# Optimization experiments

Hardware: AMD Instinct MI355X
Metric: run time of the kernel (lower is better)

## Reference

```python
import jax, jax.numpy as jnp
import numpy as np

N = 100000
E = 1600000
IN = 256
H = 4
C = 64


def setup_inputs() -> dict:
    key = jax.random.key(0)
    k1, k2, k3, k4, k5, k6 = jax.random.split(key, 6)
    x = jax.random.normal(k1, (N, IN), dtype=jnp.float32)
    edge_index = jax.random.randint(k2, (2, E), 0, N, dtype=jnp.int64)
    W = jax.random.normal(k3, (IN, H * C), dtype=jnp.float32) * (1.0 / np.sqrt(IN))
    att_src = jax.random.normal(k4, (H, C), dtype=jnp.float32) * 0.1
    att_dst = jax.random.normal(k5, (H, C), dtype=jnp.float32) * 0.1
    bias = jax.random.normal(k6, (H * C,), dtype=jnp.float32) * 0.01
    return {"x": x, "edge_index": edge_index, "W": W, "att_src": att_src, "att_dst": att_dst, "bias": bias}


def reference(x, edge_index, W, att_src, att_dst, bias):
    n = x.shape[0]
    # PyG GATConv default: add self-loops
    loops = jnp.arange(n, dtype=edge_index.dtype)
    src = jnp.concatenate([edge_index[0], loops])  # [E+N]
    dst = jnp.concatenate([edge_index[1], loops])  # [E+N]
    xp = (x @ W).reshape(n, H, C)                   # [N,H,C]
    a_src = jnp.einsum('nhc,hc->nh', xp, att_src)   # [N,H]
    a_dst = jnp.einsum('nhc,hc->nh', xp, att_dst)   # [N,H]
    # per-edge attention logits, LeakyReLU(0.2)
    alpha = jax.nn.leaky_relu(a_src[src] + a_dst[dst], negative_slope=0.2)  # [E+N,H]
    # segment softmax over destination neighborhoods (every node has a self-loop)
    amax = jax.ops.segment_max(alpha, dst, num_segments=n)
    amax = jnp.where(jnp.isfinite(amax), amax, 0.0)
    ex = jnp.exp(alpha - amax[dst])
    denom = jax.ops.segment_sum(ex, dst, num_segments=n)
    w = ex / denom[dst]                              # [E+N,H]
    # weighted scatter-add of source features
    msg = xp[src] * w[..., None]                     # [E+N,H,C]
    agg = jax.ops.segment_sum(msg, dst, num_segments=n)  # [N,H,C]
    out = agg.reshape(n, H * C) + bias
    return jax.nn.elu(out)
```

## Files before the change

### kernel.cpp

```cpp
#include <hip/hip_runtime.h>
#include <hip/hip_fp16.h>

#define FDIM 256
#define NH 4

typedef float f32x4 __attribute__((ext_vector_type(4)));
typedef short short8v __attribute__((ext_vector_type(8)));
typedef unsigned short ushort_t;
typedef unsigned short ushort8 __attribute__((ext_vector_type(8)));
typedef unsigned short ushort4v __attribute__((ext_vector_type(4)));

__device__ __forceinline__ float leaky02(float v) { return v > 0.0f ? v : 0.2f * v; }

__device__ __forceinline__ ushort_t f2bf(float f) {
    union { float f; unsigned int u; } v; v.f = f;
    unsigned int u = v.u + 0x7FFFu + ((v.u >> 16) & 1u);
    return (ushort_t)(u >> 16);
}

__device__ __forceinline__ float bf2f(ushort_t u) {
    union { float f; unsigned int u; } v;
    v.u = ((unsigned int)u) << 16;
    return v.f;
}

__device__ __forceinline__ void gload_lds16(const void* g, void* lds) {
    __builtin_amdgcn_global_load_lds((const __attribute__((address_space(1))) unsigned int*)g,
                                     (__attribute__((address_space(3))) unsigned int*)lds, 16, 0, 0);
}

__device__ __forceinline__ float recw(const int4& r, int h) {
    unsigned v = (h < 2) ? (unsigned)r.y : (unsigned)r.z;
    unsigned bits = (h & 1) ? (v >> 16) : (v & 0xFFFFu);
    __half_raw hr; hr.x = (unsigned short)bits;
    return __half2float(*reinterpret_cast<__half*>(&hr));
}

__global__ __launch_bounds__(256) void wprep_kernel(const float* __restrict__ W,
                                                    ushort_t* __restrict__ Wbf) {
    const int k = blockIdx.x;
    const int col = threadIdx.x;
    Wbf[(((size_t)(k >> 3) * 256 + col) << 3) + (k & 7)] = f2bf(W[(size_t)k * 256 + col]);
}

__global__ __launch_bounds__(512) void gemm_xp_kernel(const float* __restrict__ x,
                                                      const ushort_t* __restrict__ Wbf,
                                                      const float* __restrict__ att_s,
                                                      const float* __restrict__ att_d,
                                                      ushort_t* __restrict__ xpb,
                                                      float* __restrict__ a_src,
                                                      float* __restrict__ a_dst, int n) {
    __shared__ ushort_t a_lds[4096];
    __shared__ ushort_t b_lds[8192];
    const int t = threadIdx.x;
    const int w = t >> 6, l = t & 63;
    const int wm = w >> 2, wn = w & 3;
    const int row0 = blockIdx.x << 7;
    const int fr = l & 15, fk = l >> 4;

    const int arow = t & 127, akb = t >> 7;
    int grow = row0 + arow;
    if (grow >= n) grow = n - 1;
    const float* aptr = x + (size_t)grow * FDIM + (akb << 3);

    f32x4 acc[4][4] = {};

    for (int s = 0; s < 8; ++s) {
        float4 v0 = *(const float4*)(aptr + s * 32);
        float4 v1 = *(const float4*)(aptr + s * 32 + 4);
        ushort8 u;
        u[0]=f2bf(v0.x); u[1]=f2bf(v0.y); u[2]=f2bf(v0.z); u[3]=f2bf(v0.w);
        u[4]=f2bf(v1.x); u[5]=f2bf(v1.y); u[6]=f2bf(v1.z); u[7]=f2bf(v1.w);

        if (s) __syncthreads();

        *(ushort8*)&a_lds[(((size_t)akb << 7) + arow) << 3] = u;
        gload_lds16(Wbf + (size_t)s * 8192 + ((size_t)t << 3), (char*)b_lds + (w << 10));
        gload_lds16(Wbf + (size_t)s * 8192 + ((size_t)(t + 512) << 3), (char*)b_lds + 8192 + (w << 10));
        __syncthreads();

        short8v af[4], bfv[4];
        #pragma unroll
        for (int m = 0; m < 4; ++m)
            af[m] = *(const short8v*)&a_lds[(((size_t)fk << 7) + wm * 64 + m * 16 + fr) << 3];
        #pragma unroll
        for (int nf = 0; nf < 4; ++nf)
            bfv[nf] = *(const short8v*)&b_lds[(((size_t)fk << 8) + wn * 64 + nf * 16 + fr) << 3];
        #pragma unroll
        for (int m = 0; m < 4; ++m)
            #pragma unroll
            for (int nf = 0; nf < 4; ++nf)
                acc[m][nf] = __builtin_amdgcn_mfma_f32_16x16x32_bf16(af[m], bfv[nf], acc[m][nf], 0, 0, 0);
    }

    #pragma unroll
    for (int m = 0; m < 4; ++m) {
        const int r_ = row0 + wm * 64 + m * 16 + fk * 4;
        #pragma unroll
        for (int nf = 0; nf < 4; ++nf) {
            const int c_ = wn * 64 + nf * 16 + fr;
            #pragma unroll
            for (int j = 0; j < 4; ++j)
                if (r_ + j < n)
                    xpb[(size_t)(r_ + j) * FDIM + c_] = f2bf(acc[m][nf][j]);
        }
    }

    float att_sv[4], att_dv[4];
    #pragma unroll
    for (int nf = 0; nf < 4; ++nf) {
        att_sv[nf] = att_s[(wn << 6) + (nf << 4) + fr];
        att_dv[nf] = att_d[(wn << 6) + (nf << 4) + fr];
    }
    #pragma unroll
    for (int m = 0; m < 4; ++m) {
        #pragma unroll
        for (int j = 0; j < 4; ++j) {
            float ps = acc[m][0][j] * att_sv[0] + acc[m][1][j] * att_sv[1]
                     + acc[m][2][j] * att_sv[2] + acc[m][3][j] * att_sv[3];
            float pd = acc[m][0][j] * att_dv[0] + acc[m][1][j] * att_dv[1]
                     + acc[m][2][j] * att_dv[2] + acc[m][3][j] * att_dv[3];
            ps += __shfl_xor(ps, 1, 64); pd += __shfl_xor(pd, 1, 64);
            ps += __shfl_xor(ps, 2, 64); pd += __shfl_xor(pd, 2, 64);
            ps += __shfl_xor(ps, 4, 64); pd += __shfl_xor(pd, 4, 64);
            ps += __shfl_xor(ps, 8, 64); pd += __shfl_xor(pd, 8, 64);
            if (fr == 0) {
                const int r_ = row0 + wm * 64 + m * 16 + fk * 4 + j;
                if (r_ < n) {
                    a_src[r_ * NH + wn] = ps;
                    a_dst[r_ * NH + wn] = pd;
                }
            }
        }
    }
}

__global__ void degree_kernel(const int* __restrict__ dst, int* __restrict__ counts, int E) {
    int stride = gridDim.x * blockDim.x;
    for (int e = blockIdx.x * blockDim.x + threadIdx.x; e < E; e += stride)
        atomicAdd(&counts[dst[e]], 1);
}

__global__ __launch_bounds__(256) void scan_partial_kernel(const int* __restrict__ counts,
                                                           int* __restrict__ blockSums, int n) {
    __shared__ int sdata[256];
    const int b = blockIdx.x, t = threadIdx.x;
    const int base = b * 1024 + t * 4;
    int s = 0;
    #pragma unroll
    for (int j = 0; j < 4; ++j)
        if (base + j < n) s += counts[base + j];
    sdata[t] = s;
    __syncthreads();
    for (int off = 128; off > 0; off >>= 1) {
        if (t < off) sdata[t] += sdata[t + off];
        __syncthreads();
    }
    if (t == 0) blockSums[b] = sdata[0];
}

__global__ __launch_bounds__(256) void scan_blocksums_kernel(const int* __restrict__ blockSums,
                                                             int* __restrict__ blockOffs, int nb) {
    __shared__ int s[256];
    const int t = threadIdx.x;
    int v = (t < nb) ? blockSums[t] : 0;
    s[t] = v;
    __syncthreads();
    for (int d = 1; d < 256; d <<= 1) {
        int u = (t >= d) ? s[t - d] : 0;
        __syncthreads();
        s[t] += u;
        __syncthreads();
    }
    if (t < nb) blockOffs[t] = s[t] - v;
}

__global__ __launch_bounds__(256) void scan_final_kernel(const int* __restrict__ counts,
                                                         const int* __restrict__ blockOffs,
                                                         int* __restrict__ offsets,
                                                         int* __restrict__ cursor, int n) {
    __shared__ int s[256];
    const int b = blockIdx.x, t = threadIdx.x;
    const int base = b * 1024 + t * 4;
    int c[4];
    int tsum = 0;
    #pragma unroll
    for (int j = 0; j < 4; ++j) {
        c[j] = (base + j < n) ? counts[base + j] : 0;
        tsum += c[j];
    }
    s[t] = tsum;
    __syncthreads();
    for (int d = 1; d < 256; d <<= 1) {
        int u = (t >= d) ? s[t - d] : 0;
        __syncthreads();
        s[t] += u;
        __syncthreads();
    }
    int run = s[t] - tsum + blockOffs[b];
    #pragma unroll
    for (int j = 0; j < 4; ++j) {
        if (base + j < n) {
            offsets[base + j] = run;
            cursor[base + j] = run;
            run += c[j];
        }
    }
}

__global__ void scatter_kernel(const int* __restrict__ src, const int* __restrict__ dst,
                               const float* __restrict__ a_src, const float* __restrict__ a_dst,
                               int* __restrict__ cursor, int4* __restrict__ erec, int E) {
    int stride = gridDim.x * blockDim.x;
    for (int e = blockIdx.x * blockDim.x + threadIdx.x; e < E; e += stride) {
        const int s = src[e], d = dst[e];
        const float4 as = ((const float4*)a_src)[s];
        const float4 ad = ((const float4*)a_dst)[d];
        const float w0 = __expf(leaky02(as.x + ad.x));
        const float w1 = __expf(leaky02(as.y + ad.y));
        const float w2 = __expf(leaky02(as.z + ad.z));
        const float w3 = __expf(leaky02(as.w + ad.w));
        union { __half2 h; int i; } p01, p23;
        p01.h = __floats2half2_rn(w0, w1);
        p23.h = __floats2half2_rn(w2, w3);
        int4 rec;
        rec.x = s; rec.y = p01.i; rec.z = p23.i; rec.w = 0;
        const int pos = atomicAdd(&cursor[d], 1);
        erec[pos] = rec;
    }
}

__global__ __launch_bounds__(256) void aggregate_kernel(const ushort_t* __restrict__ xpb,
                                                        const float* __restrict__ a_src,
                                                        const float* __restrict__ a_dst,
                                                        const int* __restrict__ offsets,
                                                        const int* __restrict__ counts,
                                                        const int4* __restrict__ erec,
                                                        const float* __restrict__ bias,
                                                        float* __restrict__ out, int n) {
    const int i = (blockIdx.x << 2) + (threadIdx.x >> 6);
    if (i >= n) return;
    const int lane = threadIdx.x & 63;
    const int h = lane >> 4;
    const int start = offsets[i];
    const int cnt = counts[i];
    const int4* recs = erec + start;

    float4 acc = make_float4(0.f, 0.f, 0.f, 0.f);
    float den = 0.f;
    int e = 0;
    for (; e + 4 <= cnt; e += 4) {
        const int4 r0 = recs[e + 0];
        const int4 r1 = recs[e + 1];
        const int4 r2 = recs[e + 2];
        const int4 r3 = recs[e + 3];
        const ushort4v u0 = *(const ushort4v*)(xpb + (size_t)r0.x * FDIM + (lane << 2));
        const ushort4v u1 = *(const ushort4v*)(xpb + (size_t)r1.x * FDIM + (lane << 2));
        const ushort4v u2 = *(const ushort4v*)(xpb + (size_t)r2.x * FDIM + (lane << 2));
        const ushort4v u3 = *(const ushort4v*)(xpb + (size_t)r3.x * FDIM + (lane << 2));
        const float w0 = recw(r0, h), w1 = recw(r1, h), w2 = recw(r2, h), w3 = recw(r3, h);
        den += (w0 + w1) + (w2 + w3);
        acc.x = fmaf(w0, bf2f(u0[0]), acc.x); acc.y = fmaf(w0, bf2f(u0[1]), acc.y);
        acc.z = fmaf(w0, bf2f(u0[2]), acc.z); acc.w = fmaf(w0, bf2f(u0[3]), acc.w);
        acc.x = fmaf(w1, bf2f(u1[0]), acc.x); acc.y = fmaf(w1, bf2f(u1[1]), acc.y);
        acc.z = fmaf(w1, bf2f(u1[2]), acc.z); acc.w = fmaf(w1, bf2f(u1[3]), acc.w);
        acc.x = fmaf(w2, bf2f(u2[0]), acc.x); acc.y = fmaf(w2, bf2f(u2[1]), acc.y);
        acc.z = fmaf(w2, bf2f(u2[2]), acc.z); acc.w = fmaf(w2, bf2f(u2[3]), acc.w);
        acc.x = fmaf(w3, bf2f(u3[0]), acc.x); acc.y = fmaf(w3, bf2f(u3[1]), acc.y);
        acc.z = fmaf(w3, bf2f(u3[2]), acc.z); acc.w = fmaf(w3, bf2f(u3[3]), acc.w);
    }
    for (; e < cnt; ++e) {
        const int4 r = recs[e];
        const ushort4v u = *(const ushort4v*)(xpb + (size_t)r.x * FDIM + (lane << 2));
        const float w = recw(r, h);
        den += w;
        acc.x = fmaf(w, bf2f(u[0]), acc.x); acc.y = fmaf(w, bf2f(u[1]), acc.y);
        acc.z = fmaf(w, bf2f(u[2]), acc.z); acc.w = fmaf(w, bf2f(u[3]), acc.w);
    }
    {
        const float ws = __expf(leaky02(a_src[i * NH + h] + a_dst[i * NH + h]));
        const ushort4v u = *(const ushort4v*)(xpb + (size_t)i * FDIM + (lane << 2));
        den += ws;
        acc.x = fmaf(ws, bf2f(u[0]), acc.x); acc.y = fmaf(ws, bf2f(u[1]), acc.y);
        acc.z = fmaf(ws, bf2f(u[2]), acc.z); acc.w = fmaf(ws, bf2f(u[3]), acc.w);
    }
    const float4 b4 = ((const float4*)bias)[lane];
    float4 v;
    v.x = acc.x / den + b4.x;
    v.y = acc.y / den + b4.y;
    v.z = acc.z / den + b4.z;
    v.w = acc.w / den + b4.w;
    v.x = v.x > 0.f ? v.x : (__expf(v.x) - 1.f);
    v.y = v.y > 0.f ? v.y : (__expf(v.y) - 1.f);
    v.z = v.z > 0.f ? v.z : (__expf(v.z) - 1.f);
    v.w = v.w > 0.f ? v.w : (__expf(v.w) - 1.f);
    ((float4*)out)[(size_t)i * 64 + lane] = v;
}

extern "C" void kernel_launch(void* const* d_in, const int* in_sizes, int n_in,
                              void* d_out, int out_size, void* d_ws, size_t ws_size,
                              hipStream_t stream) {
    const float* x       = (const float*)d_in[0];
    const int*   ei      = (const int*)d_in[1];
    const float* W       = (const float*)d_in[2];
    const float* att_s   = (const float*)d_in[3];
    const float* att_d   = (const float*)d_in[4];
    const float* bias    = (const float*)d_in[5];
    float* out = (float*)d_out;

    const int n = in_sizes[0] / FDIM;
    const int E = in_sizes[1] / 2;
    const int* src = ei;
    const int* dst = ei + E;

    char* ws = (char*)d_ws;
    size_t off = 0;
    auto alloc = [&](size_t bytes) -> void* {
        void* p = ws + off;
        off = (off + bytes + 255) & ~(size_t)255;
        return p;
    };
    ushort_t* xpb  = (ushort_t*)alloc((size_t)n * FDIM * sizeof(ushort_t));
    float* a_src   = (float*)alloc((size_t)n * NH * sizeof(float));
    float* a_dst   = (float*)alloc((size_t)n * NH * sizeof(float));
    int* counts    = (int*)alloc((size_t)n * sizeof(int));
    int* offsets   = (int*)alloc((size_t)n * sizeof(int));
    int* cursor    = (int*)alloc((size_t)n * sizeof(int));
    int* blockSums = (int*)alloc(256 * sizeof(int));
    int* blockOffs = (int*)alloc(256 * sizeof(int));
    int4* erec     = (int4*)alloc((size_t)E * sizeof(int4));
    ushort_t* Wbf  = (ushort_t*)alloc((size_t)FDIM * FDIM * sizeof(ushort_t));
    (void)ws_size;

    hipMemsetAsync(counts, 0, (size_t)n * sizeof(int), stream);

    wprep_kernel<<<256, 256, 0, stream>>>(W, Wbf);
    gemm_xp_kernel<<<(n + 127) / 128, 512, 0, stream>>>(x, Wbf, att_s, att_d, xpb, a_src, a_dst, n);
    degree_kernel<<<2048, 256, 0, stream>>>(dst, counts, E);
    const int nb = (n + 1023) / 1024;
    scan_partial_kernel<<<nb, 256, 0, stream>>>(counts, blockSums, n);
    scan_blocksums_kernel<<<1, 256, 0, stream>>>(blockSums, blockOffs, nb);
    scan_final_kernel<<<nb, 256, 0, stream>>>(counts, blockOffs, offsets, cursor, n);
    scatter_kernel<<<2048, 256, 0, stream>>>(src, dst, a_src, a_dst, cursor, erec, E);
    aggregate_kernel<<<(n + 3) / 4, 256, 0, stream>>>(xpb, a_src, a_dst, offsets, counts, erec, bias, out, n);
}
```

Before: 359.1 us.

## Fuse degree counting into GEMM and split aggregation edges across half-waves

The degree atomics move out of their own kernel and into the prologue of the GEMM kernel, which removes one launch and lets the atomics overlap with GEMM work. The aggregate kernel now has each half-wavefront process alternate edges with 16-byte loads of 8 bf16 features per lane, then combines the two halves with a cross-lane shuffle. The aim is fewer, wider gather loads and more edges in flight per wave. The cost is extra shuffles and per-lane registers, and the atomics in front of the GEMM may delay its start.

```diff
diff --git a/kernel.cpp b/kernel.cpp
--- a/kernel.cpp
+++ b/kernel.cpp
@@ -8,7 +8,6 @@
 typedef short short8v __attribute__((ext_vector_type(8)));
 typedef unsigned short ushort_t;
 typedef unsigned short ushort8 __attribute__((ext_vector_type(8)));
-typedef unsigned short ushort4v __attribute__((ext_vector_type(4)));
 
 __device__ __forceinline__ float leaky02(float v) { return v > 0.0f ? v : 0.2f * v; }
 
@@ -49,10 +48,21 @@
                                                       const float* __restrict__ att_d,
                                                       ushort_t* __restrict__ xpb,
                                                       float* __restrict__ a_src,
-                                                      float* __restrict__ a_dst, int n) {
+                                                      float* __restrict__ a_dst, int n,
+                                                      const int* __restrict__ dst,
+                                                      int* __restrict__ counts, int E) {
     __shared__ ushort_t a_lds[4096];
     __shared__ ushort_t b_lds[8192];
     const int t = threadIdx.x;
+
+    {
+        const int per = (E + gridDim.x - 1) / gridDim.x;
+        const int lo = blockIdx.x * per;
+        const int hi = min(lo + per, E);
+        for (int e = lo + t; e < hi; e += 512)
+            atomicAdd(&counts[dst[e]], 1);
+    }
+
     const int w = t >> 6, l = t & 63;
     const int wm = w >> 2, wn = w & 3;
     const int row0 = blockIdx.x << 7;
@@ -133,12 +143,6 @@
             }
         }
     }
-}
-
-__global__ void degree_kernel(const int* __restrict__ dst, int* __restrict__ counts, int E) {
-    int stride = gridDim.x * blockDim.x;
-    for (int e = blockIdx.x * blockDim.x + threadIdx.x; e < E; e += stride)
-        atomicAdd(&counts[dst[e]], 1);
 }
 
 __global__ __launch_bounds__(256) void scan_partial_kernel(const int* __restrict__ counts,
@@ -241,60 +245,64 @@
     const int i = (blockIdx.x << 2) + (threadIdx.x >> 6);
     if (i >= n) return;
     const int lane = threadIdx.x & 63;
-    const int h = lane >> 4;
+    const int halfid = lane >> 5, sl = lane & 31;
+    const int h = sl >> 3;
+    const size_t colb = (size_t)sl << 3;
     const int start = offsets[i];
     const int cnt = counts[i];
     const int4* recs = erec + start;
 
-    float4 acc = make_float4(0.f, 0.f, 0.f, 0.f);
+    float acc[8] = {};
     float den = 0.f;
+
     int e = 0;
     for (; e + 4 <= cnt; e += 4) {
-        const int4 r0 = recs[e + 0];
-        const int4 r1 = recs[e + 1];
-        const int4 r2 = recs[e + 2];
-        const int4 r3 = recs[e + 3];
-        const ushort4v u0 = *(const ushort4v*)(xpb + (size_t)r0.x * FDIM + (lane << 2));
-        const ushort4v u1 = *(const ushort4v*)(xpb + (size_t)r1.x * FDIM + (lane << 2));
-        const ushort4v u2 = *(const ushort4v*)(xpb + (size_t)r2.x * FDIM + (lane << 2));
-        const ushort4v u3 = *(const ushort4v*)(xpb + (size_t)r3.x * FDIM + (lane << 2));
-        const float w0 = recw(r0, h), w1 = recw(r1, h), w2 = recw(r2, h), w3 = recw(r3, h);
-        den += (w0 + w1) + (w2 + w3);
-        acc.x = fmaf(w0, bf2f(u0[0]), acc.x); acc.y = fmaf(w0, bf2f(u0[1]), acc.y);
-        acc.z = fmaf(w0, bf2f(u0[2]), acc.z); acc.w = fmaf(w0, bf2f(u0[3]), acc.w);
-        acc.x = fmaf(w1, bf2f(u1[0]), acc.x); acc.y = fmaf(w1, bf2f(u1[1]), acc.y);
-        acc.z = fmaf(w1, bf2f(u1[2]), acc.z); acc.w = fmaf(w1, bf2f(u1[3]), acc.w);
-        acc.x = fmaf(w2, bf2f(u2[0]), acc.x); acc.y = fmaf(w2, bf2f(u2[1]), acc.y);
-        acc.z = fmaf(w2, bf2f(u2[2]), acc.z); acc.w = fmaf(w2, bf2f(u2[3]), acc.w);
-        acc.x = fmaf(w3, bf2f(u3[0]), acc.x); acc.y = fmaf(w3, bf2f(u3[1]), acc.y);
-        acc.z = fmaf(w3, bf2f(u3[2]), acc.z); acc.w = fmaf(w3, bf2f(u3[3]), acc.w);
-    }
-    for (; e < cnt; ++e) {
-        const int4 r = recs[e];
-        const ushort4v u = *(const ushort4v*)(xpb + (size_t)r.x * FDIM + (lane << 2));
-        const float w = recw(r, h);
-        den += w;
-        acc.x = fmaf(w, bf2f(u[0]), acc.x); acc.y = fmaf(w, bf2f(u[1]), acc.y);
-        acc.z = fmaf(w, bf2f(u[2]), acc.z); acc.w = fmaf(w, bf2f(u[3]), acc.w);
-    }
-    {
+        const int4 ra = recs[e + halfid];
+        const int4 rb = recs[e + 2 + halfid];
+        const ushort8 ua = *(const ushort8*)(xpb + (size_t)ra.x * FDIM + colb);
+        const ushort8 ub = *(const ushort8*)(xpb + (size_t)rb.x * FDIM + colb);
+        const float wa = recw(ra, h), wb = recw(rb, h);
+        den += wa + wb;
+        #pragma unroll
+        for (int j = 0; j < 8; ++j) acc[j] = fmaf(wa, bf2f(ua[j]), acc[j]);
+        #pragma unroll
+        for (int j = 0; j < 8; ++j) acc[j] = fmaf(wb, bf2f(ub[j]), acc[j]);
+    }
+    for (; e < cnt; e += 2) {
+        const int idx = e + halfid;
+        const int cidx = idx < cnt ? idx : cnt - 1;
+        const int4 r = recs[cidx];
+        const ushort8 u = *(const ushort8*)(xpb + (size_t)r.x * FDIM + colb);
+        const float wv = idx < cnt ? recw(r, h) : 0.f;
+        den += wv;
+        #pragma unroll
+        for (int j = 0; j < 8; ++j) acc[j] = fmaf(wv, bf2f(u[j]), acc[j]);
+    }
+    if (halfid == 0) {
         const float ws = __expf(leaky02(a_src[i * NH + h] + a_dst[i * NH + h]));
-        const ushort4v u = *(const ushort4v*)(xpb + (size_t)i * FDIM + (lane << 2));
+        const ushort8 u = *(const ushort8*)(xpb + (size_t)i * FDIM + colb);
         den += ws;
-        acc.x = fmaf(ws, bf2f(u[0]), acc.x); acc.y = fmaf(ws, bf2f(u[1]), acc.y);
-        acc.z = fmaf(ws, bf2f(u[2]), acc.z); acc.w = fmaf(ws, bf2f(u[3]), acc.w);
-    }
-    const float4 b4 = ((const float4*)bias)[lane];
+        #pragma unroll
+        for (int j = 0; j < 8; ++j) acc[j] = fmaf(ws, bf2f(u[j]), acc[j]);
+    }
+    den += __shfl_xor(den, 32, 64);
+    #pragma unroll
+    for (int j = 0; j < 8; ++j) acc[j] += __shfl_xor(acc[j], 32, 64);
+
+    const float inv = 1.0f / den;
+    const int c0 = (sl << 3) + (halfid << 2);
+    const float4 b4 = *(const float4*)(bias + c0);
+    const int jb = halfid << 2;
     float4 v;
-    v.x = acc.x / den + b4.x;
-    v.y = acc.y / den + b4.y;
-    v.z = acc.z / den + b4.z;
-    v.w = acc.w / den + b4.w;
+    v.x = acc[jb + 0] * inv + b4.x;
+    v.y = acc[jb + 1] * inv + b4.y;
+    v.z = acc[jb + 2] * inv + b4.z;
+    v.w = acc[jb + 3] * inv + b4.w;
     v.x = v.x > 0.f ? v.x : (__expf(v.x) - 1.f);
     v.y = v.y > 0.f ? v.y : (__expf(v.y) - 1.f);
     v.z = v.z > 0.f ? v.z : (__expf(v.z) - 1.f);
     v.w = v.w > 0.f ? v.w : (__expf(v.w) - 1.f);
-    ((float4*)out)[(size_t)i * 64 + lane] = v;
+    *(float4*)(out + (size_t)i * FDIM + c0) = v;
 }
 
 extern "C" void kernel_launch(void* const* d_in, const int* in_sizes, int n_in,
@@ -335,8 +343,8 @@
     hipMemsetAsync(counts, 0, (size_t)n * sizeof(int), stream);
 
     wprep_kernel<<<256, 256, 0, stream>>>(W, Wbf);
-    gemm_xp_kernel<<<(n + 127) / 128, 512, 0, stream>>>(x, Wbf, att_s, att_d, xpb, a_src, a_dst, n);
-    degree_kernel<<<2048, 256, 0, stream>>>(dst, counts, E);
+    gemm_xp_kernel<<<(n + 127) / 128, 512, 0, stream>>>(x, Wbf, att_s, att_d, xpb, a_src, a_dst, n,
+                                                        dst, counts, E);
     const int nb = (n + 1023) / 1024;
     scan_partial_kernel<<<nb, 256, 0, stream>>>(counts, blockSums, n);
     scan_blocksums_kernel<<<1, 256, 0, stream>>>(blockSums, blockOffs, nb);
```

Result: no change. 352.8 us (-1.7%).
